# Performance work log

Hardware: AMD Instinct MI355X
Metric: run time of the kernel (lower is better)

Reference implementation:

```python
import jax, jax.numpy as jnp
import numpy as np

B, C_IN, C_OUT, H, W = 16, 128, 256, 80, 80
K, STRIDE, PAD = 3, 2, 1
KK = K * K
HO = (H + 2 * PAD - K) // STRIDE + 1
WO = (W + 2 * PAD - K) // STRIDE + 1


def setup_inputs() -> dict:
    key = jax.random.key(0)
    ks = jax.random.split(key, 3)
    x = jax.random.normal(ks[0], (B, C_IN, H, W), jnp.float32)
    offset_w = jax.random.normal(ks[1], (2 * KK, C_IN), jnp.float32) * 0.01
    offset_b = jnp.zeros((2 * KK,), jnp.float32)
    deform_w = jax.random.normal(ks[2], (C_OUT, C_IN, K, K), jnp.float32) * (1.0 / np.sqrt(C_IN * KK))
    deform_b = jnp.zeros((C_OUT,), jnp.float32)
    bn_gamma = jnp.ones((C_OUT,), jnp.float32)
    bn_beta = jnp.zeros((C_OUT,), jnp.float32)
    return dict(x=x, offset_w=offset_w, offset_b=offset_b, deform_w=deform_w,
                deform_b=deform_b, bn_gamma=bn_gamma, bn_beta=bn_beta)


def _bilinear_gather(x, py, px):
    # x: [B,C,H,W]; py,px: [B,KK,HO,WO] float sample coords; zero-pad outside.
    Bb, C, Hh, Ww = x.shape
    y0 = jnp.floor(py)
    x0 = jnp.floor(px)
    wy1 = py - y0
    wx1 = px - x0
    y0i = y0.astype(jnp.int32)
    x0i = x0.astype(jnp.int32)
    flat = x.reshape(Bb, C, Hh * Ww)

    def gather(yi, xi):
        valid = (yi >= 0) & (yi < Hh) & (xi >= 0) & (xi < Ww)
        idx = jnp.clip(yi, 0, Hh - 1) * Ww + jnp.clip(xi, 0, Ww - 1)
        g = jax.vmap(lambda f, i: f[:, i])(flat, idx.reshape(Bb, -1))
        g = g.reshape(Bb, C, *yi.shape[1:])
        return g * valid[:, None].astype(x.dtype)

    g00 = gather(y0i, x0i)
    g01 = gather(y0i, x0i + 1)
    g10 = gather(y0i + 1, x0i)
    g11 = gather(y0i + 1, x0i + 1)
    wy1 = wy1[:, None]  # [B,1,KK,HO,WO]
    wx1 = wx1[:, None]
    wy0 = 1.0 - wy1
    wx0 = 1.0 - wx1
    return wy0 * (wx0 * g00 + wx1 * g01) + wy1 * (wx0 * g10 + wx1 * g11)


def reference(x, offset_w, offset_b, deform_w, deform_b, bn_gamma, bn_beta):
    Bb = x.shape[0]
    # offset conv: 1x1, stride 2 (H,W even -> simple subsample)
    xs = x[:, :, ::2, ::2]  # [B,C,HO,WO]
    off = jnp.einsum('oc,bchw->bohw', offset_w, xs) + offset_b[None, :, None, None]
    off = off.reshape(Bb, KK, 2, HO, WO)  # torchvision layout: (dy,dx) per kernel tap
    dy, dx = off[:, :, 0], off[:, :, 1]
    ky = (jnp.arange(KK) // K).astype(jnp.float32)
    kx = (jnp.arange(KK) % K).astype(jnp.float32)
    base_y = (jnp.arange(HO) * STRIDE - PAD).astype(jnp.float32)
    base_x = (jnp.arange(WO) * STRIDE - PAD).astype(jnp.float32)
    py = base_y[None, None, :, None] + ky[None, :, None, None] + dy
    px = base_x[None, None, None, :] + kx[None, :, None, None] + dx
    sampled = _bilinear_gather(x, py, px)  # [B,C,KK,HO,WO]
    w = deform_w.reshape(C_OUT, C_IN * KK)
    out = jnp.einsum('ok,bkhw->bohw', w, sampled.reshape(Bb, C_IN * KK, HO, WO))
    out = out + deform_b[None, :, None, None]
    # BatchNorm2d in training mode (batch stats, biased var, eps=1e-5)
    mean = out.mean(axis=(0, 2, 3))
    var = out.var(axis=(0, 2, 3))
    out = (out - mean[None, :, None, None]) * jax.lax.rsqrt(var + 1e-5)[None, :, None, None]
    out = out * bn_gamma[None, :, None, None] + bn_beta[None, :, None, None]
    # SiLU
    return out * jax.nn.sigmoid(out)
```

## Files before the change

kernel.cpp:

```cpp
#include <hip/hip_runtime.h>
#include <hip/hip_bf16.h>

#define B_    16
#define CIN_  128
#define COUT_ 256
#define H_    80
#define W_    80
#define HO_   40
#define WO_   40
#define KK_   9
#define SK_   1152
#define NPIX_ 25600
#define NKS_  36

typedef __attribute__((ext_vector_type(8))) short short8;
typedef __attribute__((ext_vector_type(4))) float floatx4;

__device__ __forceinline__ unsigned short f2bu(float v) {
  __hip_bfloat16 h = __float2bfloat16(v);
  return *reinterpret_cast<unsigned short*>(&h);
}
__device__ __forceinline__ float bu2f(unsigned short u) {
  return __uint_as_float(((unsigned)u) << 16);
}
__device__ __forceinline__ unsigned int pk2(float a, float b) {
  return (unsigned)f2bu(a) | ((unsigned)f2bu(b) << 16);
}
__device__ __forceinline__ void gl_lds16(const unsigned short* g, unsigned short* l) {
  __builtin_amdgcn_global_load_lds(
      (const __attribute__((address_space(1))) unsigned int*)(const void*)g,
      (__attribute__((address_space(3))) unsigned int*)(void*)l, 16, 0, 0);
}

__global__ __launch_bounds__(256) void k_pack(const float* __restrict__ dw,
                                              unsigned short* __restrict__ Apk) {
  int t = blockIdx.x * 256 + threadIdx.x;
  int j  = t & 7;
  int qd = (t >> 3) & 3;
  int m  = (t >> 5) & 255;
  int ks = t >> 13;
  int k  = ks * 32 + qd * 8 + j;
  int kk = k >> 7, ci = k & 127;
  Apk[t] = f2bu(dw[m * SK_ + ci * KK_ + kk]);
}

__global__ __launch_bounds__(256) void k_cl(const float* __restrict__ x,
                                            const float* __restrict__ ow,
                                            const float* __restrict__ ob,
                                            unsigned short* __restrict__ xcl,
                                            float* __restrict__ off) {
  __shared__ unsigned int ts[CIN_ * 41];
  __shared__ float owl[18 * CIN_];
  __shared__ float obl[18];
  const int tid = threadIdx.x;
  const int bid = blockIdx.x;
  const int xcd = bid & 7;
  const int i0_ = bid >> 3;
  const int b   = (i0_ / 80) * 8 + xcd;
  const int y   = i0_ % 80;
  const bool even = (y & 1) == 0;

  for (int j = tid; j < CIN_ * 20; j += 256) {
    int ci = j / 20, xq = j % 20;
    float4 v = *(const float4*)&x[(((size_t)b * CIN_ + ci) * H_ + y) * W_ + xq * 4];
    ts[ci * 41 + xq * 2 + 0] = pk2(v.x, v.y);
    ts[ci * 41 + xq * 2 + 1] = pk2(v.z, v.w);
  }
  if (even) {
    for (int j = tid; j < 18 * CIN_; j += 256) owl[j] = ow[j];
    if (tid < 18) obl[tid] = ob[tid];
  }
  __syncthreads();

  unsigned short* op = xcl + ((size_t)b * H_ * W_ + (size_t)y * W_) * CIN_;
  for (int j = tid; j < 40 * 32; j += 256) {
    int xw = j >> 5, cg = j & 31;
    unsigned w0 = ts[(cg * 4 + 0) * 41 + xw];
    unsigned w1 = ts[(cg * 4 + 1) * 41 + xw];
    unsigned w2 = ts[(cg * 4 + 2) * 41 + xw];
    unsigned w3 = ts[(cg * 4 + 3) * 41 + xw];
    uint2 lo = make_uint2((w0 & 0xFFFFu) | (w1 << 16),
                          (w2 & 0xFFFFu) | (w3 << 16));
    uint2 hi = make_uint2((w0 >> 16) | (w1 & 0xFFFF0000u),
                          (w2 >> 16) | (w3 & 0xFFFF0000u));
    *(uint2*)(op + (size_t)(2 * xw) * CIN_ + cg * 4)     = lo;
    *(uint2*)(op + (size_t)(2 * xw + 1) * CIN_ + cg * 4) = hi;
  }

  if (even) {
    const int ho = y >> 1;
    for (int i = tid; i < 18 * WO_; i += 256) {
      int o = i / WO_, wo = i - o * WO_;
      float acc = obl[o];
      const float* wr = &owl[o * CIN_];
#pragma unroll 4
      for (int ci = 0; ci < CIN_; ci++)
        acc += wr[ci] * bu2f((unsigned short)(ts[ci * 41 + wo] & 0xFFFFu));
      off[((b * 18 + o) * HO_ + ho) * WO_ + wo] = acc;
    }
  }
}

__global__ __launch_bounds__(256) void k_sample_cl(const unsigned short* __restrict__ xcl,
                                                   const float* __restrict__ off,
                                                   unsigned short* __restrict__ Spk) {
  __shared__ __align__(16) int   pidx[80 * 4];
  __shared__ __align__(16) float pw[80 * 4];
  const int tid = threadIdx.x;
  const int j0   = blockIdx.x;
  const int xcd  = j0 & 7;
  const int s    = j0 >> 3;
  const int b_hi = s / 180;
  const int t0   = s % 180;
  const int g    = t0 / 9;
  const int kk   = t0 % 9;
  const int b    = b_hi * 8 + xcd;
  const int ho0  = g * 2;

  if (tid < 80) {
    int hop = tid / 40, px = tid % 40;
    int ho = ho0 + hop;
    float dy = off[((b * 18 + 2 * kk) * HO_ + ho) * WO_ + px];
    float dx = off[((b * 18 + 2 * kk + 1) * HO_ + ho) * WO_ + px];
    float py  = (float)(2 * ho - 1 + (kk / 3)) + dy;
    float pxf = (float)(2 * px - 1 + (kk % 3)) + dx;
    float y0f = floorf(py), x0f = floorf(pxf);
    float wy1 = py - y0f, wx1 = pxf - x0f;
    float wy0 = 1.f - wy1, wx0 = 1.f - wx1;
    int y0 = (int)y0f, x0 = (int)x0f;
    int y1 = y0 + 1, x1 = x0 + 1;
    bool vy0 = (y0 >= 0) && (y0 < H_);
    bool vy1 = (y1 >= 0) && (y1 < H_);
    bool vx0 = (x0 >= 0) && (x0 < W_);
    bool vx1 = (x1 >= 0) && (x1 < W_);
    int y0c = min(max(y0, 0), H_ - 1), y1c = min(max(y1, 0), H_ - 1);
    int x0c = min(max(x0, 0), W_ - 1), x1c = min(max(x1, 0), W_ - 1);
    pidx[tid * 4 + 0] = (y0c * W_ + x0c) << 7;  pw[tid * 4 + 0] = (vy0 && vx0) ? wy0 * wx0 : 0.f;
    pidx[tid * 4 + 1] = (y0c * W_ + x1c) << 7;  pw[tid * 4 + 1] = (vy0 && vx1) ? wy0 * wx1 : 0.f;
    pidx[tid * 4 + 2] = (y1c * W_ + x0c) << 7;  pw[tid * 4 + 2] = (vy1 && vx0) ? wy1 * wx0 : 0.f;
    pidx[tid * 4 + 3] = (y1c * W_ + x1c) << 7;  pw[tid * 4 + 3] = (vy1 && vx1) ? wy1 * wx1 : 0.f;
  }
  __syncthreads();

  const unsigned short* xb = xcl + (size_t)b * (H_ * W_ * CIN_);
#pragma unroll
  for (int it = 0; it < 5; it++) {
    int i = it * 256 + tid;
    int oct = i & 15;
    int pxh = i >> 4;
    int4   I  = *(const int4*)&pidx[pxh * 4];
    float4 Wv = *(const float4*)&pw[pxh * 4];
    short8 c00 = *(const short8*)(xb + I.x + oct * 8);
    short8 c01 = *(const short8*)(xb + I.y + oct * 8);
    short8 c10 = *(const short8*)(xb + I.z + oct * 8);
    short8 c11 = *(const short8*)(xb + I.w + oct * 8);
    short8 r;
#pragma unroll
    for (int i2 = 0; i2 < 8; i2++) {
      float v = Wv.x * bu2f((unsigned short)c00[i2]) +
                Wv.y * bu2f((unsigned short)c01[i2]) +
                Wv.z * bu2f((unsigned short)c10[i2]) +
                Wv.w * bu2f((unsigned short)c11[i2]);
      r[i2] = (short)f2bu(v);
    }
    int p  = b * 1600 + (ho0 + (pxh / 40)) * 40 + (pxh % 40);
    int pt = p >> 4, lm = p & 15;
    int ks = kk * 4 + (oct >> 2);
    int qd = oct & 3;
    *(short8*)&Spk[(((size_t)pt * NKS_ + ks) * 64 + qd * 16 + lm) * 8] = r;
  }
}

__global__ __launch_bounds__(256) void k_gemm(const unsigned short* __restrict__ Apk,
                                              const unsigned short* __restrict__ Spk,
                                              float* __restrict__ out,
                                              float* __restrict__ accum) {
  __shared__ __align__(16) unsigned short a_sh[2][4096];
  __shared__ __align__(16) unsigned short b_sh[2][2048];

  const int tid = threadIdx.x;
  const int wv = tid >> 6;
  const int ln = tid & 63;
  const int lm = ln & 15;
  const int qd = ln >> 4;

  const int bid = blockIdx.x;
  const int xcd = bid & 7;
  const int i   = bid >> 3;
  const int b   = xcd + 8 * (i / 50);
  const int r_  = i % 50;
  const int pxg = r_ >> 1;
  const int cq  = r_ & 1;
  const int pt0 = b * 100 + pxg * 4;
  const int cbase = cq * 128;

  const unsigned short* agbase = Apk + cbase * 32 + tid * 8;
  const unsigned short* bgbase = Spk + ((size_t)(pt0 + wv) * NKS_) * 512 + ln * 8;

  floatx4 acc[8];
#pragma unroll
  for (int mt = 0; mt < 8; mt++) acc[mt] = (floatx4){0.f, 0.f, 0.f, 0.f};

  gl_lds16(agbase,        &a_sh[0][0]    + wv * 512);
  gl_lds16(agbase + 2048, &a_sh[0][2048] + wv * 512);
  gl_lds16(bgbase,        &b_sh[0][0]    + wv * 512);
  __syncthreads();

  for (int ks = 0; ks < NKS_; ks++) {
    const int buf = ks & 1, nb = buf ^ 1;
    if (ks + 1 < NKS_) {
      gl_lds16(agbase + (size_t)(ks + 1) * 8192,        &a_sh[nb][0]    + wv * 512);
      gl_lds16(agbase + (size_t)(ks + 1) * 8192 + 2048, &a_sh[nb][2048] + wv * 512);
      gl_lds16(bgbase + (size_t)(ks + 1) * 512,         &b_sh[nb][0]    + wv * 512);
    }
    const unsigned short* al = &a_sh[buf][0] + lm * 32 + qd * 8;
    short8 bv = *(const short8*)(&b_sh[buf][0] + wv * 512 + ln * 8);
#pragma unroll
    for (int mt = 0; mt < 8; mt++) {
      short8 av = *(const short8*)(al + mt * 512);
      acc[mt] = __builtin_amdgcn_mfma_f32_16x16x32_bf16(av, bv, acc[mt], 0, 0, 0);
    }
    __syncthreads();
  }

  const int p = (pt0 + wv) * 16 + lm;
  const int bb = p / 1600, rem = p % 1600;
  float* ob = out + (size_t)bb * COUT_ * 1600 + rem;
#pragma unroll
  for (int mt = 0; mt < 8; mt++) {
#pragma unroll
    for (int r = 0; r < 4; r++) {
      const int c = cbase + mt * 16 + qd * 4 + r;
      ob[(size_t)c * 1600] = acc[mt][r];
    }
  }

  float* red = (float*)&a_sh[0][0];
  red[tid < 256 ? tid : 0] = 0.f;
  __syncthreads();
#pragma unroll
  for (int mt = 0; mt < 8; mt++) {
#pragma unroll
    for (int r = 0; r < 4; r++) {
      float s = acc[mt][r];
      float q = s * s;
#pragma unroll
      for (int d = 1; d < 16; d <<= 1) {
        s += __shfl_xor(s, d, 16);
        q += __shfl_xor(q, d, 16);
      }
      if (lm == 0) {
        int lc = mt * 16 + qd * 4 + r;
        atomicAdd(&red[lc], s);
        atomicAdd(&red[128 + lc], q);
      }
    }
  }
  __syncthreads();
  if (tid < 128) {
    atomicAdd(&accum[cbase + tid],         red[tid]);
    atomicAdd(&accum[COUT_ + cbase + tid], red[128 + tid]);
  }
}

__global__ __launch_bounds__(256) void k_bn(float* __restrict__ io0,
                                            const float* __restrict__ accum,
                                            const float* __restrict__ gamma,
                                            const float* __restrict__ beta) {
  const int t = blockIdx.x * 256 + threadIdx.x;
  const int i0 = t * 4;
  const int c = (i0 / (HO_ * WO_)) % COUT_;
  const float mean = accum[c] * (1.f / NPIX_);
  const float var  = accum[COUT_ + c] * (1.f / NPIX_) - mean * mean;
  const float inv  = rsqrtf(var + 1e-5f);
  const float g  = gamma[c] * inv;
  const float be = beta[c] - mean * g;
  float4 r0 = *(const float4*)(io0 + i0);
  float v[4] = {r0.x, r0.y, r0.z, r0.w};
#pragma unroll
  for (int q = 0; q < 4; q++) {
    float u = v[q] * g + be;
    v[q] = u / (1.f + expf(-u));
  }
  *(float4*)(io0 + i0) = make_float4(v[0], v[1], v[2], v[3]);
}

extern "C" void kernel_launch(void* const* d_in, const int* in_sizes, int n_in,
                              void* d_out, int out_size, void* d_ws, size_t ws_size,
                              hipStream_t stream) {
  const float* x     = (const float*)d_in[0];
  const float* ow    = (const float*)d_in[1];
  const float* ob    = (const float*)d_in[2];
  const float* dw    = (const float*)d_in[3];
  const float* gamma = (const float*)d_in[5];
  const float* beta  = (const float*)d_in[6];
  float* out = (float*)d_out;

  float* off   = (float*)d_ws;
  float* accum = off + B_ * 18 * HO_ * WO_;
  unsigned short* Apk = (unsigned short*)(accum + 2 * COUT_);
  unsigned short* Spk = Apk + (size_t)SK_ * COUT_;
  unsigned short* xcl = Spk + (size_t)NPIX_ * SK_;

  hipMemsetAsync(accum, 0, 2 * COUT_ * sizeof(float), stream);
  k_pack<<<SK_, 256, 0, stream>>>(dw, Apk);
  k_cl<<<B_ * H_, 256, 0, stream>>>(x, ow, ob, xcl, off);
  k_sample_cl<<<B_ * KK_ * 20, 256, 0, stream>>>(xcl, off, Spk);
  k_gemm<<<800, 256, 0, stream>>>(Apk, Spk, out, accum);
  k_bn<<<(NPIX_ * COUT_ / 4 + 255) / 256, 256, 0, stream>>>(
      out, accum, gamma, beta);
}
```

Baseline: 197.9 us.

## Enlarge GEMM tile to 128x128 with 2x2 warp grid, triple buffering, swizzled LDS

Each GEMM block now covers 128 output channels by 128 pixels, with each wave owning a 64x64 sub-tile (4x4 MFMA fragments), which raises operand reuse per LDS load. The grid is halved to 400 blocks. A three-stage global-to-LDS pipeline with explicit vmcnt waits and raw s_barrier replaces the double buffer. The weight pack and sample kernels write a rotated quad-slot order so LDS reads avoid bank conflicts. The larger accumulator array raises register pressure, and 400 blocks may underfill the 256 CUs, leaving occupancy and load balance as the main risks.

Measured after the change: 185.5 us. -6.3%, faster.

```diff
diff --git a/kernel.cpp b/kernel.cpp
--- a/kernel.cpp
+++ b/kernel.cpp
@@ -36,9 +36,12 @@
                                               unsigned short* __restrict__ Apk) {
   int t = blockIdx.x * 256 + threadIdx.x;
   int j  = t & 7;
-  int qd = (t >> 3) & 3;
-  int m  = (t >> 5) & 255;
+  int sl = (t >> 3) & 3;
+  int mh = (t >> 5) & 127;
+  int cq = (t >> 12) & 1;
   int ks = t >> 13;
+  int qd = (sl - (mh >> 1)) & 3;
+  int m  = cq * 128 + mh;
   int k  = ks * 32 + qd * 8 + j;
   int kk = k >> 7, ci = k & 127;
   Apk[t] = f2bu(dw[m * SK_ + ci * KK_ + kk]);
@@ -167,7 +170,8 @@
     int pt = p >> 4, lm = p & 15;
     int ks = kk * 4 + (oct >> 2);
     int qd = oct & 3;
-    *(short8*)&Spk[(((size_t)pt * NKS_ + ks) * 64 + qd * 16 + lm) * 8] = r;
+    int gr = lm * 4 + ((qd + (lm >> 1)) & 3);
+    *(short8*)&Spk[(((size_t)pt * NKS_ + ks) * 64 + gr) * 8] = r;
   }
 }
 
@@ -175,82 +179,108 @@
                                               const unsigned short* __restrict__ Spk,
                                               float* __restrict__ out,
                                               float* __restrict__ accum) {
-  __shared__ __align__(16) unsigned short a_sh[2][4096];
-  __shared__ __align__(16) unsigned short b_sh[2][2048];
+  __shared__ __align__(16) unsigned short a_sh[3][4096];
+  __shared__ __align__(16) unsigned short b_sh[3][4096];
 
   const int tid = threadIdx.x;
   const int wv = tid >> 6;
   const int ln = tid & 63;
   const int lm = ln & 15;
   const int qd = ln >> 4;
+  const int wch = wv & 1;
+  const int wpx = wv >> 1;
 
   const int bid = blockIdx.x;
   const int xcd = bid & 7;
-  const int i   = bid >> 3;
-  const int b   = xcd + 8 * (i / 50);
-  const int r_  = i % 50;
-  const int pxg = r_ >> 1;
-  const int cq  = r_ & 1;
-  const int pt0 = b * 100 + pxg * 4;
-  const int cbase = cq * 128;
-
-  const unsigned short* agbase = Apk + cbase * 32 + tid * 8;
-  const unsigned short* bgbase = Spk + ((size_t)(pt0 + wv) * NKS_) * 512 + ln * 8;
-
-  floatx4 acc[8];
-#pragma unroll
-  for (int mt = 0; mt < 8; mt++) acc[mt] = (floatx4){0.f, 0.f, 0.f, 0.f};
-
-  gl_lds16(agbase,        &a_sh[0][0]    + wv * 512);
-  gl_lds16(agbase + 2048, &a_sh[0][2048] + wv * 512);
-  gl_lds16(bgbase,        &b_sh[0][0]    + wv * 512);
-  __syncthreads();
-
+  const int cq  = (bid >> 3) & 1;
+  const int T   = bid >> 4;
+  const int tile = T * 8 + xcd;
+  const int pt0 = tile * 8;
+
+  const unsigned short* ag = Apk + (size_t)cq * 4096 + (wv * 2) * 512 + ln * 8;
+  const unsigned short* bg0 = Spk + ((size_t)(pt0 + wv * 2 + 0) * NKS_) * 512 + ln * 8;
+  const unsigned short* bg1 = Spk + ((size_t)(pt0 + wv * 2 + 1) * NKS_) * 512 + ln * 8;
+
+#define STAGE(t, bf) do {                                                  \
+    gl_lds16(ag + (size_t)(t) * 8192,       &a_sh[bf][(wv * 2 + 0) * 512]);\
+    gl_lds16(ag + (size_t)(t) * 8192 + 512, &a_sh[bf][(wv * 2 + 1) * 512]);\
+    gl_lds16(bg0 + (size_t)(t) * 512,       &b_sh[bf][(wv * 2 + 0) * 512]);\
+    gl_lds16(bg1 + (size_t)(t) * 512,       &b_sh[bf][(wv * 2 + 1) * 512]);\
+  } while (0)
+
+  floatx4 acc[4][4];
+#pragma unroll
+  for (int mt = 0; mt < 4; mt++)
+#pragma unroll
+    for (int nt = 0; nt < 4; nt++) acc[mt][nt] = (floatx4){0.f, 0.f, 0.f, 0.f};
+
+  const int slot = (qd + (lm >> 1)) & 3;
+  const int aoff0 = (wch * 64 + lm) * 32 + slot * 8;
+  const int boff0 = (wpx * 4) * 512 + lm * 32 + slot * 8;
+
+  STAGE(0, 0);
+  STAGE(1, 1);
+  asm volatile("s_waitcnt vmcnt(4)" ::: "memory");
+  __builtin_amdgcn_s_barrier();
+
+#pragma unroll 1
   for (int ks = 0; ks < NKS_; ks++) {
-    const int buf = ks & 1, nb = buf ^ 1;
+    const int bcur = ks % 3;
+    if (ks + 2 < NKS_) STAGE(ks + 2, (ks + 2) % 3);
+
+    short8 av[4], bv[4];
+#pragma unroll
+    for (int mt = 0; mt < 4; mt++)
+      av[mt] = *(const short8*)(&a_sh[bcur][aoff0 + mt * 512]);
+#pragma unroll
+    for (int nt = 0; nt < 4; nt++)
+      bv[nt] = *(const short8*)(&b_sh[bcur][boff0 + nt * 512]);
+#pragma unroll
+    for (int mt = 0; mt < 4; mt++)
+#pragma unroll
+      for (int nt = 0; nt < 4; nt++)
+        acc[mt][nt] = __builtin_amdgcn_mfma_f32_16x16x32_bf16(av[mt], bv[nt],
+                                                              acc[mt][nt], 0, 0, 0);
     if (ks + 1 < NKS_) {
-      gl_lds16(agbase + (size_t)(ks + 1) * 8192,        &a_sh[nb][0]    + wv * 512);
-      gl_lds16(agbase + (size_t)(ks + 1) * 8192 + 2048, &a_sh[nb][2048] + wv * 512);
-      gl_lds16(bgbase + (size_t)(ks + 1) * 512,         &b_sh[nb][0]    + wv * 512);
-    }
-    const unsigned short* al = &a_sh[buf][0] + lm * 32 + qd * 8;
-    short8 bv = *(const short8*)(&b_sh[buf][0] + wv * 512 + ln * 8);
-#pragma unroll
-    for (int mt = 0; mt < 8; mt++) {
-      short8 av = *(const short8*)(al + mt * 512);
-      acc[mt] = __builtin_amdgcn_mfma_f32_16x16x32_bf16(av, bv, acc[mt], 0, 0, 0);
-    }
-    __syncthreads();
-  }
-
-  const int p = (pt0 + wv) * 16 + lm;
-  const int bb = p / 1600, rem = p % 1600;
-  float* ob = out + (size_t)bb * COUT_ * 1600 + rem;
-#pragma unroll
-  for (int mt = 0; mt < 8; mt++) {
+      if (ks < NKS_ - 2) asm volatile("s_waitcnt vmcnt(4)" ::: "memory");
+      else               asm volatile("s_waitcnt vmcnt(0)" ::: "memory");
+      __builtin_amdgcn_s_barrier();
+    }
+  }
+#undef STAGE
+
+  const int cb0 = cq * 128 + wch * 64;
+#pragma unroll
+  for (int nt = 0; nt < 4; nt++) {
+    const int p = (pt0 + wpx * 4 + nt) * 16 + lm;
+    const int bb = p / 1600, rem = p - bb * 1600;
+    float* ob = out + (size_t)bb * COUT_ * 1600 + rem;
+#pragma unroll
+    for (int mt = 0; mt < 4; mt++) {
+#pragma unroll
+      for (int r = 0; r < 4; r++)
+        ob[(size_t)(cb0 + mt * 16 + qd * 4 + r) * 1600] = acc[mt][nt][r];
+    }
+  }
+
+  __syncthreads();
+  float* red = (float*)&a_sh[0][0];
+  red[tid & 255] = 0.f;
+  __syncthreads();
+#pragma unroll
+  for (int mt = 0; mt < 4; mt++) {
 #pragma unroll
     for (int r = 0; r < 4; r++) {
-      const int c = cbase + mt * 16 + qd * 4 + r;
-      ob[(size_t)c * 1600] = acc[mt][r];
-    }
-  }
-
-  float* red = (float*)&a_sh[0][0];
-  red[tid < 256 ? tid : 0] = 0.f;
-  __syncthreads();
-#pragma unroll
-  for (int mt = 0; mt < 8; mt++) {
-#pragma unroll
-    for (int r = 0; r < 4; r++) {
-      float s = acc[mt][r];
-      float q = s * s;
+      float s = acc[mt][0][r] + acc[mt][1][r] + acc[mt][2][r] + acc[mt][3][r];
+      float q = acc[mt][0][r] * acc[mt][0][r] + acc[mt][1][r] * acc[mt][1][r] +
+                acc[mt][2][r] * acc[mt][2][r] + acc[mt][3][r] * acc[mt][3][r];
 #pragma unroll
       for (int d = 1; d < 16; d <<= 1) {
         s += __shfl_xor(s, d, 16);
         q += __shfl_xor(q, d, 16);
       }
       if (lm == 0) {
-        int lc = mt * 16 + qd * 4 + r;
+        int lc = wch * 64 + mt * 16 + qd * 4 + r;
         atomicAdd(&red[lc], s);
         atomicAdd(&red[128 + lc], q);
       }
@@ -258,8 +288,8 @@
   }
   __syncthreads();
   if (tid < 128) {
-    atomicAdd(&accum[cbase + tid],         red[tid]);
-    atomicAdd(&accum[COUT_ + cbase + tid], red[128 + tid]);
+    atomicAdd(&accum[cq * 128 + tid],         red[tid]);
+    atomicAdd(&accum[COUT_ + cq * 128 + tid], red[128 + tid]);
   }
 }
 
@@ -306,7 +336,7 @@
   k_pack<<<SK_, 256, 0, stream>>>(dw, Apk);
   k_cl<<<B_ * H_, 256, 0, stream>>>(x, ow, ob, xcl, off);
   k_sample_cl<<<B_ * KK_ * 20, 256, 0, stream>>>(xcl, off, Spk);
-  k_gemm<<<800, 256, 0, stream>>>(Apk, Spk, out, accum);
+  k_gemm<<<400, 256, 0, stream>>>(Apk, Spk, out, accum);
   k_bn<<<(NPIX_ * COUT_ / 4 + 255) / 256, 256, 0, stream>>>(
       out, accum, gamma, beta);
 }
```
